# Optimization experiments

Measured on AMD Instinct MI355X. Metric: run time of the kernel, lower is better.

Reference implementation:

```python
import jax, jax.numpy as jnp
import numpy as np

D_MODEL = 1024
NUM_HEADS = 16
BATCH = 2
SEQ = 2048


def _trunc_normal(key, shape, std):
    # truncated normal on [-3std, 3std], matching torch.nn.init.trunc_normal_
    return jax.random.truncated_normal(key, -3.0, 3.0, shape, dtype=jnp.float32) * std


def setup_inputs() -> dict:
    key = jax.random.key(0)
    kx, kq, kk, kv, ko = jax.random.split(key, 5)
    std = (2.0 / (D_MODEL + D_MODEL)) ** 0.5
    return {
        "X": jax.random.normal(kx, (BATCH, SEQ, D_MODEL), dtype=jnp.float32),
        "q_proj": _trunc_normal(kq, (D_MODEL, D_MODEL), std),
        "k_proj": _trunc_normal(kk, (D_MODEL, D_MODEL), std),
        "v_proj": _trunc_normal(kv, (D_MODEL, D_MODEL), std),
        "o_proj": _trunc_normal(ko, (D_MODEL, D_MODEL), std),
    }


def reference(X, q_proj, k_proj, v_proj, o_proj):
    B, S, D = X.shape
    H = NUM_HEADS
    d_k = D // H

    # weights stored as (d_model, d_model); split output dim into heads
    q_w = q_proj.reshape(H, d_k, D)        # heads d_k d_model
    k_w = k_proj.reshape(H, d_k, D)
    v_w = v_proj.reshape(H, d_k, D)
    o_w = o_proj.reshape(D, H, d_k).transpose(1, 0, 2)  # heads d_model d_v

    q = jnp.einsum('hkd,bsd->bhsk', q_w, X)  # [B,H,S,d_k]
    k = jnp.einsum('hkd,bsd->bhsk', k_w, X)
    v = jnp.einsum('hkd,bsd->bhsk', v_w, X)

    scale = 1.0 / jnp.sqrt(jnp.asarray(d_k, dtype=X.dtype))
    scores = jnp.einsum('bhqk,bhsk->bhqs', q, k) * scale  # [B,H,S,S]
    causal = jnp.tril(jnp.ones((S, S), dtype=bool))
    scores = jnp.where(causal, scores, jnp.asarray(-jnp.inf, dtype=scores.dtype))
    attn = jax.nn.softmax(scores, axis=-1)
    attn_out = jnp.einsum('bhqs,bhsk->bhqk', attn, v)  # [B,H,S,d_v]

    return jnp.einsum('hdv,bhsv->bsd', o_w, attn_out)  # [B,S,d_model]
```

## Files before the change

### kernel.cpp

```cpp
#include <hip/hip_runtime.h>

typedef unsigned short u16;
typedef __bf16 bf16x8 __attribute__((ext_vector_type(8)));
typedef float f32x4 __attribute__((ext_vector_type(4)));
typedef u16 u16x8 __attribute__((ext_vector_type(8)));
typedef u16 u16x4v __attribute__((ext_vector_type(4)));

#define D_MODEL 1024
#define SEQ 2048
#define NB 2
#define NH 16

#define MFMA(a, b, c) __builtin_amdgcn_mfma_f32_16x16x32_bf16(a, b, c, 0, 0, 0)

__device__ __forceinline__ u16 f2bf(float f) {
  unsigned u = __builtin_bit_cast(unsigned, f);
  u += 0x7FFFu + ((u >> 16) & 1u);
  return (u16)(u >> 16);
}

__device__ __forceinline__ u16 f2bf_hw(float f) {
  return __builtin_bit_cast(u16, (__bf16)f);
}

__device__ __forceinline__ bf16x8 ld8(const u16* p) {
  return __builtin_bit_cast(bf16x8, *(const u16x8*)p);
}

typedef const __attribute__((address_space(1))) unsigned gu32;
typedef __attribute__((address_space(3))) unsigned lu32;
__device__ __forceinline__ void gload16(const u16* g, u16* l) {
  __builtin_amdgcn_global_load_lds((gu32*)g, (lu32*)l, 16, 0, 0);
}

#define WAITV8 asm volatile("s_waitcnt vmcnt(8)" ::: "memory")
#define WAITV4 asm volatile("s_waitcnt vmcnt(4)" ::: "memory")
#define WAITV0 asm volatile("s_waitcnt vmcnt(0)" ::: "memory")
#define BARRIER __builtin_amdgcn_s_barrier()
#define SB0 __builtin_amdgcn_sched_barrier(0)

__global__ __launch_bounds__(256) void convert_kernel(
    const float* __restrict__ X, const float* __restrict__ Wq,
    const float* __restrict__ Wk, const float* __restrict__ Wv,
    const float* __restrict__ Wo, u16* __restrict__ Xb, u16* __restrict__ Wb)
{
  const int NX4 = 1024 * 1024;
  const int NW4 = 256 * 1024;
  const int TOT = NX4 + 4 * NW4;
  for (int i = blockIdx.x * 256 + threadIdx.x; i < TOT; i += gridDim.x * 256) {
    const float* src;
    u16* dst;
    if (i < NX4) {
      src = X + (size_t)i * 4;
      dst = Xb + (size_t)i * 4;
    } else {
      int j = i - NX4;
      int w = j >> 18;
      int off = j & (NW4 - 1);
      const float* ws = (w == 0) ? Wq : (w == 1) ? Wk : (w == 2) ? Wv : Wo;
      src = ws + (size_t)off * 4;
      dst = Wb + (size_t)j * 4;
    }
    float4 v = *(const float4*)src;
    u16x4v o = { f2bf(v.x), f2bf(v.y), f2bf(v.z), f2bf(v.w) };
    *(u16x4v*)dst = o;
  }
}

__global__ __launch_bounds__(512, 2) void qkv8w(
    const u16* __restrict__ A, const u16* __restrict__ B,
    u16* __restrict__ Qb, u16* __restrict__ Kb, u16* __restrict__ Vt)
{
  __shared__ u16 As[4][8192];
  __shared__ u16 Bs[4][8192];
  const int t = threadIdx.x;
  const int lane = t & 63, w = t >> 6;
  const int wm = w >> 2, wn = w & 3;
  const int m0 = blockIdx.x * 256;
  const int n0 = blockIdx.y * 256;
  const int kg = lane >> 4, lr = lane & 15;
  const int rp = lr >> 1, hf = lr & 1;
  const int xr = (((hf * 4 + kg) ^ rp) * 8);

  const int lc = (lane & 7) ^ (lane >> 3);
  const int ghalf = lc >> 2, kc = lc & 3;

  f32x4 acc[8][4] = {};

  auto stage = [&](int buf, int kt) {
    #pragma unroll
    for (int j = 0; j < 2; ++j) {
      int g = (j * 64 + w * 8 + (lane >> 3)) * 2 + ghalf;
      gload16(&A[(size_t)(m0 + g) * 1024 + kt * 32 + kc * 8],
              &As[buf][(j * 8 + w) * 512]);
      gload16(&B[(size_t)(n0 + g) * 1024 + kt * 32 + kc * 8],
              &Bs[buf][(j * 8 + w) * 512]);
    }
  };

  auto phase = [&](int buf) {
    const u16* as = &As[buf][0];
    const u16* bs = &Bs[buf][0];
    bf16x8 a[8], b[4];
    #pragma unroll
    for (int mi = 0; mi < 8; ++mi)
      a[mi] = ld8(&as[(wm * 64 + mi * 8 + rp) * 64 + xr]);
    #pragma unroll
    for (int ni = 0; ni < 4; ++ni)
      b[ni] = ld8(&bs[(wn * 32 + ni * 8 + rp) * 64 + xr]);
    __builtin_amdgcn_s_setprio(1);
    #pragma unroll
    for (int mi = 0; mi < 8; ++mi)
      #pragma unroll
      for (int ni = 0; ni < 4; ++ni)
        acc[mi][ni] = MFMA(a[mi], b[ni], acc[mi][ni]);
    __builtin_amdgcn_s_setprio(0);
  };

  stage(0, 0);
  stage(1, 1);
  stage(2, 2);

  for (int tt = 0; tt < 28; tt += 4) {
    #pragma unroll
    for (int q = 0; q < 4; ++q) {
      const int kt = tt + q;
      WAITV8;
      BARRIER;
      SB0;
      stage((q + 3) & 3, kt + 3);
      phase(q);
    }
  }
  WAITV8; BARRIER; SB0; stage(3, 31); phase(0);
  WAITV8; BARRIER; SB0; phase(1);
  WAITV4; BARRIER; SB0; phase(2);
  WAITV0; BARRIER; SB0; phase(3);

  const int zby = blockIdx.y >> 2;
  const int nl0 = (blockIdx.y & 3) * 256;
  const float scl = (zby == 0) ? 0.125f : 1.0f;
  #pragma unroll
  for (int mi = 0; mi < 8; ++mi) {
    #pragma unroll
    for (int ni = 0; ni < 4; ++ni) {
      int m = m0 + wm * 128 + mi * 16 + kg * 4;
      int nl = nl0 + wn * 64 + ni * 16 + lr;
      int bb = m >> 11, s = m & (SEQ - 1);
      int h = nl >> 6, dk = nl & 63;
      size_t bh = (size_t)(bb * NH + h);
      if (zby == 2) {
        u16x4v v = { f2bf(acc[mi][ni][0]), f2bf(acc[mi][ni][1]),
                     f2bf(acc[mi][ni][2]), f2bf(acc[mi][ni][3]) };
        *(u16x4v*)&Vt[(bh * 64 + dk) * SEQ + s] = v;
      } else {
        u16* dst = (zby == 0 ? Qb : Kb) + ((bh * SEQ + s) * 64 + dk);
        #pragma unroll
        for (int i = 0; i < 4; ++i) dst[(size_t)i * 64] = f2bf(acc[mi][ni][i] * scl);
      }
    }
  }
}

__global__ __launch_bounds__(256) void oproj_kernel(
    const u16* __restrict__ A, const u16* __restrict__ B,
    float* __restrict__ out)
{
  __shared__ u16 As[2][128 * 64];
  __shared__ u16 Bs[2][128 * 64];
  const int t = threadIdx.x;
  const int lane = t & 63, w = t >> 6;
  const int wr = w >> 1, wc = w & 1;
  const int m0 = blockIdx.x * 128;
  const int n0 = blockIdx.y * 128;
  const int kg = lane >> 4, lr = lane & 15;
  const int lrow = lane >> 3, lch = lane & 7;

  f32x4 acc[4][4] = {};

  auto stage = [&](int buf, int kt) {
    #pragma unroll
    for (int i = 0; i < 4; ++i) {
      int row = (w * 4 + i) * 8 + lrow;
      int sch = lch ^ (row & 7);
      gload16(&A[(size_t)(m0 + row) * 1024 + kt * 64 + sch * 8], &As[buf][(w * 4 + i) * 512]);
      gload16(&B[(size_t)(n0 + row) * 1024 + kt * 64 + sch * 8], &Bs[buf][(w * 4 + i) * 512]);
    }
  };

  stage(0, 0);
  __syncthreads();
  int cur = 0;

  for (int kt = 0; kt < 16; ++kt) {
    if (kt + 1 < 16) stage(cur ^ 1, kt + 1);

    const u16* as = &As[cur][0];
    const u16* bs = &Bs[cur][0];
    #pragma unroll
    for (int kh = 0; kh < 2; ++kh) {
      bf16x8 a[4], b[4];
      #pragma unroll
      for (int mi = 0; mi < 4; ++mi) {
        int row = wr * 64 + mi * 16 + lr;
        int ch = (kh * 4 + kg) ^ (lr & 7);
        a[mi] = ld8(&as[row * 64 + ch * 8]);
      }
      #pragma unroll
      for (int ni = 0; ni < 4; ++ni) {
        int row = wc * 64 + ni * 16 + lr;
        int ch = (kh * 4 + kg) ^ (lr & 7);
        b[ni] = ld8(&bs[row * 64 + ch * 8]);
      }
      #pragma unroll
      for (int mi = 0; mi < 4; ++mi)
        #pragma unroll
        for (int ni = 0; ni < 4; ++ni)
          acc[mi][ni] = MFMA(a[mi], b[ni], acc[mi][ni]);
    }

    __syncthreads();
    cur ^= 1;
  }

  #pragma unroll
  for (int mi = 0; mi < 4; ++mi) {
    #pragma unroll
    for (int ni = 0; ni < 4; ++ni) {
      int m = m0 + wr * 64 + mi * 16 + kg * 4;
      int n = n0 + wc * 64 + ni * 16 + lr;
      #pragma unroll
      for (int i = 0; i < 4; ++i)
        out[(size_t)(m + i) * D_MODEL + n] = acc[mi][ni][i];
    }
  }
}

__global__ __launch_bounds__(256) void attn_kernel(
    const u16* __restrict__ Qb, const u16* __restrict__ Kb,
    const u16* __restrict__ Vt, u16* __restrict__ AO)
{
  __shared__ u16 Ks[2][64 * 64];
  __shared__ u16 Vs[2][64 * 64];
  __shared__ u16 Ps[4][16][72];
  const int t = threadIdx.x;
  const int bh = blockIdx.x;
  const int p = blockIdx.y;
  const int lane = t & 63, wv = t >> 6;
  const int kg = lane >> 4, lr = lane & 15;
  const int r8 = lane >> 3, c = lane & 7;
  const int b = bh >> 4, h = bh & (NH - 1);

  auto stage = [&](int buf, int kv0) {
    #pragma unroll
    for (int i = 0; i < 2; ++i) {
      int s = wv * 2 + i;
      int row = s * 8 + r8;
      int sc = c ^ (row & 7);
      gload16(&Kb[((size_t)bh * SEQ + kv0 + row) * 64 + sc * 8], &Ks[buf][s * 512]);
      gload16(&Vt[((size_t)bh * 64 + row) * SEQ + kv0 + sc * 8], &Vs[buf][s * 512]);
    }
  };

  #pragma unroll 1
  for (int seg = 0; seg < 2; ++seg) {
    const int qt = seg ? (31 - p) : p;
    const int ntile = qt + 1;
    const int q0 = qt * 64;

    const size_t qrow = (size_t)bh * SEQ + q0 + wv * 16 + lr;
    bf16x8 aq0 = ld8(&Qb[qrow * 64 + kg * 8]);
    bf16x8 aq1 = ld8(&Qb[qrow * 64 + 32 + kg * 8]);

    f32x4 of[4] = {};
    float rs[4] = {0.f, 0.f, 0.f, 0.f};

    __syncthreads();
    stage(0, 0);
    int cur = 0;

    for (int kt = 0; kt < ntile; ++kt) {
      const int kv0 = kt * 64;
      __syncthreads();
      if (kt + 1 < ntile) stage(cur ^ 1, (kt + 1) * 64);

      const u16* kb = &Ks[cur][0];
      f32x4 sc4[4] = {};
      __builtin_amdgcn_s_setprio(1);
      #pragma unroll
      for (int ct = 0; ct < 4; ++ct) {
        int ch0 = kg ^ (lr & 7);
        int ch1 = (4 + kg) ^ (lr & 7);
        sc4[ct] = MFMA(aq0, ld8(&kb[(ct * 16 + lr) * 64 + ch0 * 8]), sc4[ct]);
        sc4[ct] = MFMA(aq1, ld8(&kb[(ct * 16 + lr) * 64 + ch1 * 8]), sc4[ct]);
      }
      __builtin_amdgcn_s_setprio(0);

      const bool domask = (kt == ntile - 1);
      #pragma unroll
      for (int ct = 0; ct < 4; ++ct)
        #pragma unroll
        for (int i = 0; i < 4; ++i) {
          float e = __expf(sc4[ct][i]);
          if (domask && (kv0 + ct * 16 + lr > q0 + wv * 16 + kg * 4 + i)) e = 0.f;
          sc4[ct][i] = e;
          rs[i] += e;
        }

      #pragma unroll
      for (int ct = 0; ct < 4; ++ct)
        #pragma unroll
        for (int i = 0; i < 4; ++i)
          Ps[wv][kg * 4 + i][ct * 16 + lr] = f2bf_hw(sc4[ct][i]);

      bf16x8 pa0 = ld8(&Ps[wv][lr][kg * 8]);
      bf16x8 pa1 = ld8(&Ps[wv][lr][32 + kg * 8]);

      const u16* vb = &Vs[cur][0];
      __builtin_amdgcn_s_setprio(1);
      #pragma unroll
      for (int vt = 0; vt < 4; ++vt) {
        int ch0 = kg ^ (lr & 7);
        int ch1 = (4 + kg) ^ (lr & 7);
        of[vt] = MFMA(pa0, ld8(&vb[(vt * 16 + lr) * 64 + ch0 * 8]), of[vt]);
        of[vt] = MFMA(pa1, ld8(&vb[(vt * 16 + lr) * 64 + ch1 * 8]), of[vt]);
      }
      __builtin_amdgcn_s_setprio(0);
      cur ^= 1;
    }

    #pragma unroll
    for (int off = 1; off < 16; off <<= 1)
      #pragma unroll
      for (int i = 0; i < 4; ++i)
        rs[i] += __shfl_xor(rs[i], off, 64);

    #pragma unroll
    for (int i = 0; i < 4; ++i) {
      float inv = 1.0f / rs[i];
      int s = q0 + wv * 16 + kg * 4 + i;
      size_t base = ((size_t)(b * SEQ + s)) * D_MODEL + h * 64 + lr;
      #pragma unroll
      for (int vt = 0; vt < 4; ++vt)
        AO[base + vt * 16] = f2bf_hw(of[vt][i] * inv);
    }
  }
}

extern "C" void kernel_launch(void* const* d_in, const int* in_sizes, int n_in,
                              void* d_out, int out_size, void* d_ws, size_t ws_size,
                              hipStream_t stream) {
  const float* X  = (const float*)d_in[0];
  const float* Wq = (const float*)d_in[1];
  const float* Wk = (const float*)d_in[2];
  const float* Wv = (const float*)d_in[3];
  const float* Wo = (const float*)d_in[4];
  float* out = (float*)d_out;

  u16* Xb = (u16*)d_ws;
  u16* Wb = Xb + (size_t)4096 * 1024;
  u16* Qb = Wb + (size_t)4096 * 1024;
  u16* Kb = Qb + (size_t)4096 * 1024;
  u16* Vt = Kb + (size_t)4096 * 1024;
  u16* AO = Vt + (size_t)4096 * 1024;

  convert_kernel<<<2048, 256, 0, stream>>>(X, Wq, Wk, Wv, Wo, Xb, Wb);
  qkv8w<<<dim3(16, 12), 512, 0, stream>>>(Xb, Wb, Qb, Kb, Vt);
  attn_kernel<<<dim3(32, 16), 256, 0, stream>>>(Qb, Kb, Vt, AO);
  oproj_kernel<<<dim3(32, 8), 256, 0, stream>>>(AO, Wb + (size_t)3 * 1024 * 1024, out);
}
```

Measured before the change: 110.2 us.

## Widen attention KV tile to 128 and split K/V staging with explicit waits

The attention kernel now processes 128 keys per iteration instead of 64, which halves the number of loop iterations and barriers per query tile. K stays double-buffered, while V moves to a single XOR-swizzled buffer that is loaded separately. Partial vmcnt waits let the QK^T matmul and softmax overlap with the V load. The cost is a larger LDS footprint (about 65 KB per block), which may lower occupancy. On the diagonal, masking now wastes up to 64 extra key columns of compute.

```diff
diff --git a/kernel.cpp b/kernel.cpp
--- a/kernel.cpp
+++ b/kernel.cpp
@@ -240,33 +240,43 @@
     const u16* __restrict__ Qb, const u16* __restrict__ Kb,
     const u16* __restrict__ Vt, u16* __restrict__ AO)
 {
-  __shared__ u16 Ks[2][64 * 64];
-  __shared__ u16 Vs[2][64 * 64];
-  __shared__ u16 Ps[4][16][72];
+  __shared__ u16 Ks[2][128 * 64];
+  __shared__ u16 Vs[64 * 128];
+  __shared__ u16 Ps[4][16][132];
   const int t = threadIdx.x;
   const int bh = blockIdx.x;
   const int p = blockIdx.y;
   const int lane = t & 63, wv = t >> 6;
   const int kg = lane >> 4, lr = lane & 15;
-  const int r8 = lane >> 3, c = lane & 7;
   const int b = bh >> 4, h = bh & (NH - 1);
 
-  auto stage = [&](int buf, int kv0) {
-    #pragma unroll
-    for (int i = 0; i < 2; ++i) {
-      int s = wv * 2 + i;
-      int row = s * 8 + r8;
-      int sc = c ^ (row & 7);
-      gload16(&Kb[((size_t)bh * SEQ + kv0 + row) * 64 + sc * 8], &Ks[buf][s * 512]);
-      gload16(&Vt[((size_t)bh * 64 + row) * SEQ + kv0 + sc * 8], &Vs[buf][s * 512]);
+  const int kr8 = lane >> 3, kc = lane & 7;
+  const int vr4 = lane >> 4, vc = lane & 15;
+
+  auto stageK = [&](int buf, int kv0) {
+    #pragma unroll
+    for (int j = 0; j < 4; ++j) {
+      int r = (wv * 4 + j) * 8 + kr8;
+      int lc = kc ^ (r & 7);
+      gload16(&Kb[((size_t)bh * SEQ + kv0 + r) * 64 + lc * 8],
+              &Ks[buf][(wv * 4 + j) * 512]);
+    }
+  };
+  auto stageV = [&](int kv0) {
+    #pragma unroll
+    for (int j = 0; j < 4; ++j) {
+      int r = (wv * 4 + j) * 4 + vr4;
+      int lc = vc ^ (r & 15);
+      gload16(&Vt[((size_t)bh * 64 + r) * SEQ + kv0 + lc * 8],
+              &Vs[(wv * 4 + j) * 512]);
     }
   };
 
   #pragma unroll 1
   for (int seg = 0; seg < 2; ++seg) {
     const int qt = seg ? (31 - p) : p;
-    const int ntile = qt + 1;
     const int q0 = qt * 64;
+    const int ntile = (qt >> 1) + 1;
 
     const size_t qrow = (size_t)bh * SEQ + q0 + wv * 16 + lr;
     bf16x8 aq0 = ld8(&Qb[qrow * 64 + kg * 8]);
@@ -276,55 +286,66 @@
     float rs[4] = {0.f, 0.f, 0.f, 0.f};
 
     __syncthreads();
-    stage(0, 0);
+    stageK(0, 0);
     int cur = 0;
 
+    #pragma unroll 1
     for (int kt = 0; kt < ntile; ++kt) {
-      const int kv0 = kt * 64;
-      __syncthreads();
-      if (kt + 1 < ntile) stage(cur ^ 1, (kt + 1) * 64);
+      const int kv0 = kt * 128;
+      const bool last = (kt + 1 == ntile);
+
+      WAITV0;
+      BARRIER;
+      SB0;
+      stageV(kv0);
+      if (!last) stageK(cur ^ 1, kv0 + 128);
 
       const u16* kb = &Ks[cur][0];
-      f32x4 sc4[4] = {};
+      f32x4 sc8[8] = {};
       __builtin_amdgcn_s_setprio(1);
       #pragma unroll
-      for (int ct = 0; ct < 4; ++ct) {
+      for (int ct = 0; ct < 8; ++ct) {
         int ch0 = kg ^ (lr & 7);
         int ch1 = (4 + kg) ^ (lr & 7);
-        sc4[ct] = MFMA(aq0, ld8(&kb[(ct * 16 + lr) * 64 + ch0 * 8]), sc4[ct]);
-        sc4[ct] = MFMA(aq1, ld8(&kb[(ct * 16 + lr) * 64 + ch1 * 8]), sc4[ct]);
+        sc8[ct] = MFMA(aq0, ld8(&kb[(ct * 16 + lr) * 64 + ch0 * 8]), sc8[ct]);
+        sc8[ct] = MFMA(aq1, ld8(&kb[(ct * 16 + lr) * 64 + ch1 * 8]), sc8[ct]);
       }
       __builtin_amdgcn_s_setprio(0);
 
-      const bool domask = (kt == ntile - 1);
-      #pragma unroll
-      for (int ct = 0; ct < 4; ++ct)
+      const bool domask = last;
+      #pragma unroll
+      for (int ct = 0; ct < 8; ++ct)
         #pragma unroll
         for (int i = 0; i < 4; ++i) {
-          float e = __expf(sc4[ct][i]);
+          float e = __expf(sc8[ct][i]);
           if (domask && (kv0 + ct * 16 + lr > q0 + wv * 16 + kg * 4 + i)) e = 0.f;
-          sc4[ct][i] = e;
+          sc8[ct][i] = e;
           rs[i] += e;
         }
 
       #pragma unroll
-      for (int ct = 0; ct < 4; ++ct)
+      for (int ct = 0; ct < 8; ++ct)
         #pragma unroll
         for (int i = 0; i < 4; ++i)
-          Ps[wv][kg * 4 + i][ct * 16 + lr] = f2bf_hw(sc4[ct][i]);
-
-      bf16x8 pa0 = ld8(&Ps[wv][lr][kg * 8]);
-      bf16x8 pa1 = ld8(&Ps[wv][lr][32 + kg * 8]);
-
-      const u16* vb = &Vs[cur][0];
+          Ps[wv][kg * 4 + i][ct * 16 + lr] = f2bf_hw(sc8[ct][i]);
+
+      bf16x8 pa[4];
+      #pragma unroll
+      for (int ks = 0; ks < 4; ++ks)
+        pa[ks] = ld8(&Ps[wv][lr][ks * 32 + kg * 8]);
+
+      if (last) { WAITV0; } else { WAITV4; }
+      BARRIER;
+      SB0;
+
       __builtin_amdgcn_s_setprio(1);
       #pragma unroll
-      for (int vt = 0; vt < 4; ++vt) {
-        int ch0 = kg ^ (lr & 7);
-        int ch1 = (4 + kg) ^ (lr & 7);
-        of[vt] = MFMA(pa0, ld8(&vb[(vt * 16 + lr) * 64 + ch0 * 8]), of[vt]);
-        of[vt] = MFMA(pa1, ld8(&vb[(vt * 16 + lr) * 64 + ch1 * 8]), of[vt]);
-      }
+      for (int vt = 0; vt < 4; ++vt)
+        #pragma unroll
+        for (int ks = 0; ks < 4; ++ks) {
+          int ch = (ks * 4 + kg) ^ lr;
+          of[vt] = MFMA(pa[ks], ld8(&Vs[(vt * 16 + lr) * 128 + ch * 8]), of[vt]);
+        }
       __builtin_amdgcn_s_setprio(0);
       cur ^= 1;
     }
```

Measured after the change: 119.9 us. 1.09x slower.
